# Optimization experiments

Hardware: AMD Instinct MI355X
Metric: run time of the kernel (lower is better)

The kernel has to match this reference:

```python
import jax, jax.numpy as jnp
import numpy as np


def _gcn_conv(x, W, b, src, dst, norm, n_nodes):
    # PyG GCNConv: h = x @ W, then symmetric-normalized aggregation, then + b
    h = x @ W                                   # [N, F_out]
    msg = h[src] * norm[:, None]                # gather + scale, [E', F_out]
    agg = jax.ops.segment_sum(msg, dst, num_segments=n_nodes)
    return agg + b


def _norm_and_loops(edge_index, n_nodes):
    # add self-loops, compute D^{-1/2} (A+I) D^{-1/2} edge weights
    loop = jnp.arange(n_nodes, dtype=edge_index.dtype)
    src = jnp.concatenate([edge_index[0], loop])
    dst = jnp.concatenate([edge_index[1], loop])
    deg = jax.ops.segment_sum(jnp.ones_like(dst, dtype=jnp.float32), dst,
                              num_segments=n_nodes)
    dinv = jnp.where(deg > 0, jax.lax.rsqrt(deg), 0.0)
    norm = dinv[src] * dinv[dst]
    return src, dst, norm


def setup_inputs() -> dict:
    key = jax.random.key(0)
    ks = jax.random.split(key, 4)
    N, E, n_latent, n_dim = 50000, 800000, 128, 128
    hidden = 2 * n_latent
    x = jax.random.normal(ks[0], (N, n_latent), dtype=jnp.float32)
    edge_index = jax.random.randint(ks[1], (2, E), 0, N, dtype=jnp.int64)
    W1 = jax.random.normal(ks[2], (n_latent, hidden), dtype=jnp.float32) / np.sqrt(n_latent)
    b1 = jnp.zeros((hidden,), dtype=jnp.float32)
    W2 = jax.random.normal(ks[3], (hidden, n_dim), dtype=jnp.float32) / np.sqrt(hidden)
    b2 = jnp.zeros((n_dim,), dtype=jnp.float32)
    return {"x": x, "edge_index": edge_index, "W1": W1, "b1": b1,
            "W2": W2, "b2": b2}


def reference(x, edge_index, W1, b1, W2, b2):
    n_nodes = x.shape[0]
    src, dst, norm = _norm_and_loops(edge_index, n_nodes)
    z1 = jax.nn.relu(_gcn_conv(x, W1, b1, src, dst, norm, n_nodes))
    z2 = _gcn_conv(z1, W2, b2, src, dst, norm, n_nodes)
    return z2
```

## Files before the change

kernel.cpp:

```cpp
#include <hip/hip_runtime.h>


constexpr int F = 128;
constexpr int HID = 256;
constexpr int ECHUNK = 8192;

typedef __attribute__((ext_vector_type(8))) _Float16 f16x8;
typedef __attribute__((ext_vector_type(4))) _Float16 f16x4;
typedef __attribute__((ext_vector_type(4))) float f32x4;

__global__ __launch_bounds__(256) void k_prep(const int* __restrict__ dst,
                                              unsigned* __restrict__ bcnt,
                                              unsigned* __restrict__ bhist,
                                              const float* __restrict__ W1,
                                              const float* __restrict__ W2,
                                              const float* __restrict__ x,
                                              _Float16* __restrict__ w1t,
                                              _Float16* __restrict__ w2t,
                                              _Float16* __restrict__ xh,
                                              int E, int nbC, int n4) {
  __shared__ unsigned hist[256];
  int b = blockIdx.x;
  int tid = threadIdx.x;
  if (b < nbC) {
    hist[tid] = 0u;
    __syncthreads();
    int i0 = b * ECHUNK;
    int i1 = min(i0 + ECHUNK, E);
    for (int i = i0 + tid; i < i1; i += 256)
      atomicAdd(&hist[((unsigned)dst[i]) >> 8], 1u);
    __syncthreads();
    unsigned c = hist[tid];
    bhist[b * 256 + tid] = c;
    if (c) atomicAdd(&bcnt[tid], c);
  } else if (b < nbC + 128) {
    int idx = (b - nbC) * 256 + tid;
    int k = idx / HID, n = idx - k * HID;
    w1t[n * F + k] = (_Float16)W1[idx];
  } else if (b < nbC + 256) {
    int idx = (b - nbC - 128) * 256 + tid;
    int k = idx / F, n = idx - k * F;
    w2t[n * HID + k] = (_Float16)W2[idx];
  } else {
    int i = (b - nbC - 256) * 256 + tid;
    if (i < n4) {
      float4 v = ((const float4*)x)[i];
      f16x4 o;
      o.x = (_Float16)v.x; o.y = (_Float16)v.y;
      o.z = (_Float16)v.z; o.w = (_Float16)v.w;
      ((f16x4*)xh)[i] = o;
    }
  }
}

__global__ __launch_bounds__(256) void k_bscan(const unsigned* __restrict__ bcnt,
                                               unsigned* __restrict__ bbase,
                                               unsigned* __restrict__ bcur,
                                               int* __restrict__ rowptr,
                                               int P, int N, int E) {
  __shared__ unsigned wsum[4];
  int tid = threadIdx.x;
  unsigned v = (tid < P) ? bcnt[tid] : 0u;
  unsigned sv = v;
#pragma unroll
  for (int off = 1; off < 64; off <<= 1) {
    unsigned t = __shfl_up(sv, off);
    if ((tid & 63) >= off) sv += t;
  }
  int w = tid >> 6;
  if ((tid & 63) == 63) wsum[w] = sv;
  __syncthreads();
  unsigned wpre = 0;
  for (int k = 0; k < w; ++k) wpre += wsum[k];
  unsigned excl = wpre + sv - v;
  if (tid < P) {
    bbase[tid] = excl;
    bcur[tid] = excl;
  }
  if (tid == P - 1) bbase[P] = excl + v;
  if (tid == 0) rowptr[N] = E;
}

__global__ __launch_bounds__(256) void k_binscat(const int* __restrict__ src,
                                                 const int* __restrict__ dst,
                                                 const unsigned* __restrict__ bhist,
                                                 unsigned* __restrict__ bcur,
                                                 unsigned* __restrict__ packed, int E) {
  __shared__ unsigned hist[256];
  __shared__ unsigned basel[256];
  int tid = threadIdx.x;
  unsigned c = bhist[blockIdx.x * 256 + tid];
  if (c) basel[tid] = atomicAdd(&bcur[tid], c);
  hist[tid] = 0u;
  __syncthreads();
  int i0 = blockIdx.x * ECHUNK;
  int i1 = min(i0 + ECHUNK, E);
  for (int i = i0 + tid; i < i1; i += 256) {
    unsigned d = (unsigned)dst[i];
    unsigned b = d >> 8;
    unsigned pos = basel[b] + atomicAdd(&hist[b], 1u);
    packed[pos] = ((unsigned)src[i]) | ((d & 255u) << 16);
  }
}

__global__ __launch_bounds__(256) void k_bcsr(const unsigned* __restrict__ packed,
                                              const unsigned* __restrict__ bbase,
                                              float* __restrict__ dinv,
                                              int* __restrict__ rowptr,
                                              int* __restrict__ esrc, int N) {
  __shared__ unsigned hist[256];
  __shared__ unsigned rowloc[256];
  __shared__ unsigned cur[256];
  __shared__ unsigned wsum[4];
  int tid = threadIdx.x, b = blockIdx.x;
  int e0 = (int)bbase[b], e1 = (int)bbase[b + 1];
  hist[tid] = 0u;
  __syncthreads();
  for (int i = e0 + tid; i < e1; i += 256)
    atomicAdd(&hist[packed[i] >> 16], 1u);
  __syncthreads();
  unsigned v = hist[tid];
  unsigned sv = v;
#pragma unroll
  for (int off = 1; off < 64; off <<= 1) {
    unsigned t = __shfl_up(sv, off);
    if ((tid & 63) >= off) sv += t;
  }
  int w = tid >> 6;
  if ((tid & 63) == 63) wsum[w] = sv;
  __syncthreads();
  unsigned wpre = 0;
  for (int k = 0; k < w; ++k) wpre += wsum[k];
  unsigned excl = wpre + sv - v;
  int node = b * 256 + tid;
  if (node < N) {
    dinv[node] = rsqrtf((float)v + 1.0f);
    rowptr[node] = e0 + (int)excl;
  }
  rowloc[tid] = (unsigned)e0 + excl;
  cur[tid] = 0u;
  __syncthreads();
  for (int i = e0 + tid; i < e1; i += 256) {
    unsigned pk = packed[i];
    unsigned dl = pk >> 16;
    unsigned pos = rowloc[dl] + atomicAdd(&cur[dl], 1u);
    esrc[pos] = (int)(pk & 0xffffu);
  }
}

__global__ __launch_bounds__(256) void k_agg1(const int* __restrict__ rowptr,
                                              const int* __restrict__ esrc,
                                              const float* __restrict__ dinv,
                                              const _Float16* __restrict__ xh,
                                              _Float16* __restrict__ outp, int N) {
  int node = blockIdx.x * 16 + (threadIdx.x >> 4);
  int li = threadIdx.x & 15;
  int lanebase = (threadIdx.x & 63) & 48;
  if (node >= N) return;
  float di = dinv[node];
  float w0 = di * di;
  f16x8 svv = ((const f16x8*)(xh + (size_t)node * F))[li];
  float acc[8] = {};
  int beg = rowptr[node], end = rowptr[node + 1];
  for (int b = beg; b < end; b += 16) {
    int n = min(16, end - b);
    int s = 0;
    float w = 0.f;
    if (li < n) {
      s = esrc[b + li];
      w = dinv[s] * di;
    }
    int t = 0;
    for (; t + 7 < n; t += 8) {
      int ss[8];
      float wz[8];
#pragma unroll
      for (int j = 0; j < 8; ++j) {
        ss[j] = __shfl(s, lanebase + t + j);
        wz[j] = __shfl(w, lanebase + t + j);
      }
      f16x8 vv[8];
#pragma unroll
      for (int j = 0; j < 8; ++j)
        vv[j] = ((const f16x8*)(xh + (size_t)ss[j] * F))[li];
#pragma unroll
      for (int j = 0; j < 8; ++j)
#pragma unroll
        for (int k = 0; k < 8; ++k)
          acc[k] += (float)vv[j][k] * wz[j];
    }
    for (; t + 3 < n; t += 4) {
      int ss[4];
      float wz[4];
#pragma unroll
      for (int j = 0; j < 4; ++j) {
        ss[j] = __shfl(s, lanebase + t + j);
        wz[j] = __shfl(w, lanebase + t + j);
      }
      f16x8 vv[4];
#pragma unroll
      for (int j = 0; j < 4; ++j)
        vv[j] = ((const f16x8*)(xh + (size_t)ss[j] * F))[li];
#pragma unroll
      for (int j = 0; j < 4; ++j)
#pragma unroll
        for (int k = 0; k < 8; ++k)
          acc[k] += (float)vv[j][k] * wz[j];
    }
    for (; t < n; ++t) {
      int s0 = __shfl(s, lanebase + t);
      float wa = __shfl(w, lanebase + t);
      f16x8 v0 = ((const f16x8*)(xh + (size_t)s0 * F))[li];
#pragma unroll
      for (int k = 0; k < 8; ++k) acc[k] += (float)v0[k] * wa;
    }
  }
  f16x8 ov;
#pragma unroll
  for (int k = 0; k < 8; ++k) ov[k] = (_Float16)(acc[k] + (float)svv[k] * w0);
  ((f16x8*)(outp + (size_t)node * F))[li] = ov;
}

__global__ __launch_bounds__(256) void k_agg_out(const int* __restrict__ rowptr,
                                                 const int* __restrict__ esrc,
                                                 const float* __restrict__ dinv,
                                                 const _Float16* __restrict__ hb,
                                                 const float* __restrict__ bias,
                                                 float* __restrict__ outp, int N) {
  int node = blockIdx.x * 16 + (threadIdx.x >> 4);
  int li = threadIdx.x & 15;
  int lanebase = (threadIdx.x & 63) & 48;
  if (node >= N) return;
  float di = dinv[node];
  float w0 = di * di;
  f16x8 svv = ((const f16x8*)(hb + (size_t)node * F))[li];
  float acc[8] = {};
  int beg = rowptr[node], end = rowptr[node + 1];
  for (int b = beg; b < end; b += 16) {
    int n = min(16, end - b);
    int s = 0;
    float w = 0.f;
    if (li < n) {
      s = esrc[b + li];
      w = dinv[s] * di;
    }
    int t = 0;
    for (; t + 7 < n; t += 8) {
      int ss[8];
      float wz[8];
#pragma unroll
      for (int j = 0; j < 8; ++j) {
        ss[j] = __shfl(s, lanebase + t + j);
        wz[j] = __shfl(w, lanebase + t + j);
      }
      f16x8 vv[8];
#pragma unroll
      for (int j = 0; j < 8; ++j)
        vv[j] = ((const f16x8*)(hb + (size_t)ss[j] * F))[li];
#pragma unroll
      for (int j = 0; j < 8; ++j)
#pragma unroll
        for (int k = 0; k < 8; ++k)
          acc[k] += (float)vv[j][k] * wz[j];
    }
    for (; t + 3 < n; t += 4) {
      int ss[4];
      float wz[4];
#pragma unroll
      for (int j = 0; j < 4; ++j) {
        ss[j] = __shfl(s, lanebase + t + j);
        wz[j] = __shfl(w, lanebase + t + j);
      }
      f16x8 vv[4];
#pragma unroll
      for (int j = 0; j < 4; ++j)
        vv[j] = ((const f16x8*)(hb + (size_t)ss[j] * F))[li];
#pragma unroll
      for (int j = 0; j < 4; ++j)
#pragma unroll
        for (int k = 0; k < 8; ++k)
          acc[k] += (float)vv[j][k] * wz[j];
    }
    for (; t < n; ++t) {
      int s0 = __shfl(s, lanebase + t);
      float wa = __shfl(w, lanebase + t);
      f16x8 v0 = ((const f16x8*)(hb + (size_t)s0 * F))[li];
#pragma unroll
      for (int k = 0; k < 8; ++k) acc[k] += (float)v0[k] * wa;
    }
  }
  float4 bb0 = ((const float4*)bias)[li * 2];
  float4 bb1 = ((const float4*)bias)[li * 2 + 1];
  float4 o0, o1;
  o0.x = acc[0] + (float)svv[0] * w0 + bb0.x;
  o0.y = acc[1] + (float)svv[1] * w0 + bb0.y;
  o0.z = acc[2] + (float)svv[2] * w0 + bb0.z;
  o0.w = acc[3] + (float)svv[3] * w0 + bb0.w;
  o1.x = acc[4] + (float)svv[4] * w0 + bb1.x;
  o1.y = acc[5] + (float)svv[5] * w0 + bb1.y;
  o1.z = acc[6] + (float)svv[6] * w0 + bb1.z;
  o1.w = acc[7] + (float)svv[7] * w0 + bb1.w;
  float* orow = outp + (size_t)node * F + li * 8;
  *(float4*)orow = o0;
  *(float4*)(orow + 4) = o1;
}

__global__ __launch_bounds__(256) void k_gemm1(const _Float16* __restrict__ A,
                                               const _Float16* __restrict__ Bt,
                                               const float* __restrict__ bias,
                                               _Float16* __restrict__ C, int M) {
  __shared__ _Float16 AL[64 * 128];
  int tid = threadIdx.x;
  int lane = tid & 63, wid = tid >> 6;
  int row0 = blockIdx.x * 64;

#pragma unroll
  for (int i = 0; i < 4; ++i) {
    int g = i * 256 + tid;
    int r = g >> 4, gi = g & 15;
    int o = r * 128 + ((gi ^ (r & 7)) * 8);
    size_t go = (size_t)(row0 + r) * 128 + gi * 8;
    *(f16x8*)&AL[o] = *(const f16x8*)&A[go];
  }
  __syncthreads();

  f32x4 acc[4][4] = {};
#pragma unroll
  for (int ks = 0; ks < 4; ++ks) {
    f16x8 ah[4], bh[4];
#pragma unroll
    for (int mf = 0; mf < 4; ++mf) {
      int r = mf * 16 + (lane & 15);
      int g = ks * 4 + (lane >> 4);
      int o = r * 128 + ((g ^ (r & 7)) * 8);
      ah[mf] = *(const f16x8*)&AL[o];
    }
#pragma unroll
    for (int nf = 0; nf < 4; ++nf) {
      int c = wid * 64 + nf * 16 + (lane & 15);
      size_t o = (size_t)c * 128 + ks * 32 + (lane >> 4) * 8;
      bh[nf] = *(const f16x8*)&Bt[o];
    }
#pragma unroll
    for (int mf = 0; mf < 4; ++mf)
#pragma unroll
      for (int nf = 0; nf < 4; ++nf)
        acc[mf][nf] = __builtin_amdgcn_mfma_f32_16x16x32_f16(
            ah[mf], bh[nf], acc[mf][nf], 0, 0, 0);
  }

#pragma unroll
  for (int mf = 0; mf < 4; ++mf) {
    int r0 = row0 + mf * 16 + (lane >> 4) * 4;
#pragma unroll
    for (int nf = 0; nf < 4; ++nf) {
      int c = wid * 64 + nf * 16 + (lane & 15);
      float bv = bias[c];
#pragma unroll
      for (int r = 0; r < 4; ++r) {
        if (r0 + r < M) {
          float v = fmaxf(acc[mf][nf][r] + bv, 0.f);
          C[(size_t)(r0 + r) * HID + c] = (_Float16)v;
        }
      }
    }
  }
}

__global__ __launch_bounds__(256) void k_gemm2(const _Float16* __restrict__ Z,
                                               const _Float16* __restrict__ Bt,
                                               _Float16* __restrict__ C, int M) {
  __shared__ _Float16 ZL[64 * 256];
  int tid = threadIdx.x;
  int lane = tid & 63, wid = tid >> 6;
  int row0 = blockIdx.x * 64;

#pragma unroll
  for (int i = 0; i < 8; ++i) {
    int g = i * 256 + tid;
    int r = g >> 5, gi = g & 31;
    int o = r * 256 + ((gi ^ (r & 7)) * 8);
    size_t go = (size_t)(row0 + r) * 256 + gi * 8;
    *(f16x8*)&ZL[o] = *(const f16x8*)&Z[go];
  }
  __syncthreads();

  f32x4 acc[4][2] = {};
#pragma unroll
  for (int ks = 0; ks < 8; ++ks) {
    f16x8 ah[4], bh[2];
#pragma unroll
    for (int mf = 0; mf < 4; ++mf) {
      int r = mf * 16 + (lane & 15);
      int g = ks * 4 + (lane >> 4);
      int o = r * 256 + ((g ^ (r & 7)) * 8);
      ah[mf] = *(const f16x8*)&ZL[o];
    }
#pragma unroll
    for (int nf = 0; nf < 2; ++nf) {
      int c = wid * 32 + nf * 16 + (lane & 15);
      size_t o = (size_t)c * 256 + ks * 32 + (lane >> 4) * 8;
      bh[nf] = *(const f16x8*)&Bt[o];
    }
#pragma unroll
    for (int mf = 0; mf < 4; ++mf)
#pragma unroll
      for (int nf = 0; nf < 2; ++nf)
        acc[mf][nf] = __builtin_amdgcn_mfma_f32_16x16x32_f16(
            ah[mf], bh[nf], acc[mf][nf], 0, 0, 0);
  }

#pragma unroll
  for (int mf = 0; mf < 4; ++mf) {
    int r0 = row0 + mf * 16 + (lane >> 4) * 4;
#pragma unroll
    for (int nf = 0; nf < 2; ++nf) {
      int c = wid * 32 + nf * 16 + (lane & 15);
#pragma unroll
      for (int r = 0; r < 4; ++r)
        if (r0 + r < M) C[(size_t)(r0 + r) * F + c] = (_Float16)acc[mf][nf][r];
    }
  }
}

extern "C" void kernel_launch(void* const* d_in, const int* in_sizes, int n_in,
                              void* d_out, int out_size, void* d_ws, size_t ws_size,
                              hipStream_t stream) {
  const float* x = (const float*)d_in[0];
  const int* ei = (const int*)d_in[1];
  const float* W1 = (const float*)d_in[2];
  const float* b1 = (const float*)d_in[3];
  const float* W2 = (const float*)d_in[4];
  const float* b2 = (const float*)d_in[5];
  float* out = (float*)d_out;

  int N = in_sizes[0] / F;
  int E = in_sizes[1] / 2;
  const int* src = ei;
  const int* dst = ei + E;
  int P = (N + 255) / 256;
  int nbC = (E + ECHUNK - 1) / ECHUNK;

  char* ws = (char*)d_ws;
  size_t off = 0;
  auto allocB = [&](size_t bytes) {
    void* p = ws + off;
    off += ((bytes + 255) & ~(size_t)255);
    return p;
  };
  float* dinv = (float*)allocB((size_t)N * 4);
  int* rowptr = (int*)allocB(((size_t)N + 1) * 4);
  unsigned* bcnt = (unsigned*)allocB(256 * 4);
  unsigned* bbase = (unsigned*)allocB(257 * 4);
  unsigned* bcur = (unsigned*)allocB(256 * 4);
  unsigned* bhist = (unsigned*)allocB((size_t)nbC * 256 * 4);
  unsigned* packed = (unsigned*)allocB((size_t)E * 4);
  int* esrc = (int*)allocB((size_t)E * 4);
  _Float16* xh = (_Float16*)allocB((size_t)N * F * 2);
  _Float16* agg = (_Float16*)allocB((size_t)(N + 64) * F * 2);
  _Float16* z1 = (_Float16*)allocB((size_t)(N + 64) * HID * 2);
  _Float16* w1t = (_Float16*)allocB((size_t)F * HID * 2);
  _Float16* w2t = (_Float16*)allocB((size_t)HID * F * 2);
  _Float16* h2 = agg;

  int n4 = N * F / 4;
  int nbPrep = nbC + 256 + (n4 + 255) / 256;

  hipMemsetAsync(bcnt, 0, 256 * 4, stream);
  k_prep<<<nbPrep, 256, 0, stream>>>(dst, bcnt, bhist, W1, W2, x, w1t, w2t, xh,
                                     E, nbC, n4);
  k_bscan<<<1, 256, 0, stream>>>(bcnt, bbase, bcur, rowptr, P, N, E);
  k_binscat<<<nbC, 256, 0, stream>>>(src, dst, bhist, bcur, packed, E);
  k_bcsr<<<P, 256, 0, stream>>>(packed, bbase, dinv, rowptr, esrc, N);

  int nbAgg = (N + 15) / 16;
  int mb = (N + 63) / 64;

  k_agg1<<<nbAgg, 256, 0, stream>>>(rowptr, esrc, dinv, xh, agg, N);
  k_gemm1<<<mb, 256, 0, stream>>>(agg, w1t, b1, z1, N);

  k_gemm2<<<mb, 256, 0, stream>>>(z1, w2t, h2, N);
  k_agg_out<<<nbAgg, 256, 0, stream>>>(rowptr, esrc, dinv, h2, b2, out, N);
}
```

Measured before the change: 168.8 us.

## Fuse the two GEMMs through LDS and drop the global bucket-count atomics

The two dense layers are merged into one kernel. The ReLU'd hidden activations z1 now stay in a swizzled LDS tile and feed the second MFMA GEMM directly, instead of making a round trip through global memory. This removes the z1 buffer and one kernel launch, at the cost of more LDS per block (48 KB total). Separately, the per-bucket totals are now computed in the single-block scan by summing the per-chunk histograms, which removes the memset and the global atomics in the prep kernel but adds a serial loop in the scan. Row bounds checks are dropped because the agg buffer is padded by 64 rows.

```diff
diff --git a/kernel.cpp b/kernel.cpp
--- a/kernel.cpp
+++ b/kernel.cpp
@@ -10,7 +10,6 @@
 typedef __attribute__((ext_vector_type(4))) float f32x4;
 
 __global__ __launch_bounds__(256) void k_prep(const int* __restrict__ dst,
-                                              unsigned* __restrict__ bcnt,
                                               unsigned* __restrict__ bhist,
                                               const float* __restrict__ W1,
                                               const float* __restrict__ W2,
@@ -30,9 +29,7 @@
     for (int i = i0 + tid; i < i1; i += 256)
       atomicAdd(&hist[((unsigned)dst[i]) >> 8], 1u);
     __syncthreads();
-    unsigned c = hist[tid];
-    bhist[b * 256 + tid] = c;
-    if (c) atomicAdd(&bcnt[tid], c);
+    bhist[b * 256 + tid] = hist[tid];
   } else if (b < nbC + 128) {
     int idx = (b - nbC) * 256 + tid;
     int k = idx / HID, n = idx - k * HID;
@@ -53,14 +50,17 @@
   }
 }
 
-__global__ __launch_bounds__(256) void k_bscan(const unsigned* __restrict__ bcnt,
+__global__ __launch_bounds__(256) void k_bscan(const unsigned* __restrict__ bhist,
+                                               int nbC,
                                                unsigned* __restrict__ bbase,
                                                unsigned* __restrict__ bcur,
                                                int* __restrict__ rowptr,
                                                int P, int N, int E) {
   __shared__ unsigned wsum[4];
   int tid = threadIdx.x;
-  unsigned v = (tid < P) ? bcnt[tid] : 0u;
+  unsigned v = 0u;
+  for (int c = 0; c < nbC; ++c) v += bhist[c * 256 + tid];
+  if (tid >= P) v = 0u;
   unsigned sv = v;
 #pragma unroll
   for (int off = 1; off < 64; off <<= 1) {
@@ -305,11 +305,13 @@
   *(float4*)(orow + 4) = o1;
 }
 
-__global__ __launch_bounds__(256) void k_gemm1(const _Float16* __restrict__ A,
-                                               const _Float16* __restrict__ Bt,
+__global__ __launch_bounds__(256) void k_fgemm(const _Float16* __restrict__ A,
+                                               const _Float16* __restrict__ B1,
                                                const float* __restrict__ bias,
-                                               _Float16* __restrict__ C, int M) {
+                                               const _Float16* __restrict__ B2,
+                                               _Float16* __restrict__ H2, int M) {
   __shared__ _Float16 AL[64 * 128];
+  __shared__ _Float16 ZL[64 * 256];
   int tid = threadIdx.x;
   int lane = tid & 63, wid = tid >> 6;
   int row0 = blockIdx.x * 64;
@@ -332,14 +334,12 @@
     for (int mf = 0; mf < 4; ++mf) {
       int r = mf * 16 + (lane & 15);
       int g = ks * 4 + (lane >> 4);
-      int o = r * 128 + ((g ^ (r & 7)) * 8);
-      ah[mf] = *(const f16x8*)&AL[o];
+      ah[mf] = *(const f16x8*)&AL[r * 128 + ((g ^ (r & 7)) * 8)];
     }
 #pragma unroll
     for (int nf = 0; nf < 4; ++nf) {
       int c = wid * 64 + nf * 16 + (lane & 15);
-      size_t o = (size_t)c * 128 + ks * 32 + (lane >> 4) * 8;
-      bh[nf] = *(const f16x8*)&Bt[o];
+      bh[nf] = *(const f16x8*)&B1[(size_t)c * 128 + ks * 32 + (lane >> 4) * 8];
     }
 #pragma unroll
     for (int mf = 0; mf < 4; ++mf)
@@ -351,41 +351,23 @@
 
 #pragma unroll
   for (int mf = 0; mf < 4; ++mf) {
-    int r0 = row0 + mf * 16 + (lane >> 4) * 4;
+    int r0l = mf * 16 + (lane >> 4) * 4;
 #pragma unroll
     for (int nf = 0; nf < 4; ++nf) {
       int c = wid * 64 + nf * 16 + (lane & 15);
       float bv = bias[c];
+      int gi = c >> 3, ci = c & 7;
 #pragma unroll
       for (int r = 0; r < 4; ++r) {
-        if (r0 + r < M) {
-          float v = fmaxf(acc[mf][nf][r] + bv, 0.f);
-          C[(size_t)(r0 + r) * HID + c] = (_Float16)v;
-        }
+        int rr = r0l + r;
+        float v = fmaxf(acc[mf][nf][r] + bv, 0.f);
+        ZL[rr * 256 + ((gi ^ (rr & 7)) * 8) + ci] = (_Float16)v;
       }
     }
   }
-}
-
-__global__ __launch_bounds__(256) void k_gemm2(const _Float16* __restrict__ Z,
-                                               const _Float16* __restrict__ Bt,
-                                               _Float16* __restrict__ C, int M) {
-  __shared__ _Float16 ZL[64 * 256];
-  int tid = threadIdx.x;
-  int lane = tid & 63, wid = tid >> 6;
-  int row0 = blockIdx.x * 64;
-
-#pragma unroll
-  for (int i = 0; i < 8; ++i) {
-    int g = i * 256 + tid;
-    int r = g >> 5, gi = g & 31;
-    int o = r * 256 + ((gi ^ (r & 7)) * 8);
-    size_t go = (size_t)(row0 + r) * 256 + gi * 8;
-    *(f16x8*)&ZL[o] = *(const f16x8*)&Z[go];
-  }
-  __syncthreads();
-
-  f32x4 acc[4][2] = {};
+  __syncthreads();
+
+  f32x4 acc2[4][2] = {};
 #pragma unroll
   for (int ks = 0; ks < 8; ++ks) {
     f16x8 ah[4], bh[2];
@@ -393,21 +375,19 @@
     for (int mf = 0; mf < 4; ++mf) {
       int r = mf * 16 + (lane & 15);
       int g = ks * 4 + (lane >> 4);
-      int o = r * 256 + ((g ^ (r & 7)) * 8);
-      ah[mf] = *(const f16x8*)&ZL[o];
+      ah[mf] = *(const f16x8*)&ZL[r * 256 + ((g ^ (r & 7)) * 8)];
     }
 #pragma unroll
     for (int nf = 0; nf < 2; ++nf) {
       int c = wid * 32 + nf * 16 + (lane & 15);
-      size_t o = (size_t)c * 256 + ks * 32 + (lane >> 4) * 8;
-      bh[nf] = *(const f16x8*)&Bt[o];
+      bh[nf] = *(const f16x8*)&B2[(size_t)c * 256 + ks * 32 + (lane >> 4) * 8];
     }
 #pragma unroll
     for (int mf = 0; mf < 4; ++mf)
 #pragma unroll
       for (int nf = 0; nf < 2; ++nf)
-        acc[mf][nf] = __builtin_amdgcn_mfma_f32_16x16x32_f16(
-            ah[mf], bh[nf], acc[mf][nf], 0, 0, 0);
+        acc2[mf][nf] = __builtin_amdgcn_mfma_f32_16x16x32_f16(
+            ah[mf], bh[nf], acc2[mf][nf], 0, 0, 0);
   }
 
 #pragma unroll
@@ -418,7 +398,7 @@
       int c = wid * 32 + nf * 16 + (lane & 15);
 #pragma unroll
       for (int r = 0; r < 4; ++r)
-        if (r0 + r < M) C[(size_t)(r0 + r) * F + c] = (_Float16)acc[mf][nf][r];
+        H2[(size_t)(r0 + r) * F + c] = (_Float16)acc2[mf][nf][r];
     }
   }
 }
@@ -450,7 +430,6 @@
   };
   float* dinv = (float*)allocB((size_t)N * 4);
   int* rowptr = (int*)allocB(((size_t)N + 1) * 4);
-  unsigned* bcnt = (unsigned*)allocB(256 * 4);
   unsigned* bbase = (unsigned*)allocB(257 * 4);
   unsigned* bcur = (unsigned*)allocB(256 * 4);
   unsigned* bhist = (unsigned*)allocB((size_t)nbC * 256 * 4);
@@ -458,7 +437,6 @@
   int* esrc = (int*)allocB((size_t)E * 4);
   _Float16* xh = (_Float16*)allocB((size_t)N * F * 2);
   _Float16* agg = (_Float16*)allocB((size_t)(N + 64) * F * 2);
-  _Float16* z1 = (_Float16*)allocB((size_t)(N + 64) * HID * 2);
   _Float16* w1t = (_Float16*)allocB((size_t)F * HID * 2);
   _Float16* w2t = (_Float16*)allocB((size_t)HID * F * 2);
   _Float16* h2 = agg;
@@ -466,10 +444,9 @@
   int n4 = N * F / 4;
   int nbPrep = nbC + 256 + (n4 + 255) / 256;
 
-  hipMemsetAsync(bcnt, 0, 256 * 4, stream);
-  k_prep<<<nbPrep, 256, 0, stream>>>(dst, bcnt, bhist, W1, W2, x, w1t, w2t, xh,
+  k_prep<<<nbPrep, 256, 0, stream>>>(dst, bhist, W1, W2, x, w1t, w2t, xh,
                                      E, nbC, n4);
-  k_bscan<<<1, 256, 0, stream>>>(bcnt, bbase, bcur, rowptr, P, N, E);
+  k_bscan<<<1, 256, 0, stream>>>(bhist, nbC, bbase, bcur, rowptr, P, N, E);
   k_binscat<<<nbC, 256, 0, stream>>>(src, dst, bhist, bcur, packed, E);
   k_bcsr<<<P, 256, 0, stream>>>(packed, bbase, dinv, rowptr, esrc, N);
 
@@ -477,8 +454,6 @@
   int mb = (N + 63) / 64;
 
   k_agg1<<<nbAgg, 256, 0, stream>>>(rowptr, esrc, dinv, xh, agg, N);
-  k_gemm1<<<mb, 256, 0, stream>>>(agg, w1t, b1, z1, N);
-
-  k_gemm2<<<mb, 256, 0, stream>>>(z1, w2t, h2, N);
+  k_fgemm<<<mb, 256, 0, stream>>>(agg, w1t, b1, w2t, h2, N);
   k_agg_out<<<nbAgg, 256, 0, stream>>>(rowptr, esrc, dinv, h2, b2, out, N);
 }
```

New measurement: 160.4 us. 5.0% less time.
